# Kernel optimization log

Measured on AMD Instinct MI355X. Metric: run time of the kernel, lower is better.

## Reference

```python
import jax, jax.numpy as jnp
import numpy as np

EPS = 1e-5
NUM_GROUPS = 32
NUM_HEADS = 8

def group_norm(x, w, b):
    # x: (B, C, H, W), 32 groups, affine per-channel
    B, C, H, W = x.shape
    xg = x.reshape(B, NUM_GROUPS, C // NUM_GROUPS, H, W)
    mu = xg.mean(axis=(2, 3, 4), keepdims=True)
    var = xg.var(axis=(2, 3, 4), keepdims=True)
    xn = ((xg - mu) * jax.lax.rsqrt(var + EPS)).reshape(B, C, H, W)
    return xn * w[None, :, None, None] + b[None, :, None, None]

def conv1x1(x, w, b):
    # 1x1 conv == per-pixel linear; w: (out, in), x: (B, C, H, W)
    return jnp.einsum('oc,bchw->bohw', w, x) + b[None, :, None, None]

def setup_inputs() -> dict:
    key = jax.random.key(0)
    ks = jax.random.split(key, 4)
    B, C, H, W = 2, 512, 64, 64
    s = 1.0 / np.sqrt(C)
    return {
        'x': jax.random.normal(ks[0], (B, C, H, W), jnp.float32),
        'gn_w': jnp.ones((C,), jnp.float32),
        'gn_b': jnp.zeros((C,), jnp.float32),
        'wq': jax.random.normal(ks[1], (C, C), jnp.float32) * s,
        'bq': jnp.zeros((C,), jnp.float32),
        'wkv': jax.random.normal(ks[2], (2 * C, C), jnp.float32) * s,
        'bkv': jnp.zeros((2 * C,), jnp.float32),
        'wo': jax.random.normal(ks[3], (C, C), jnp.float32) * s,
        'bo': jnp.zeros((C,), jnp.float32),
    }

def reference(x, gn_w, gn_b, wq, bq, wkv, bkv, wo, bo):
    B, C, H, W = x.shape
    hd = C // NUM_HEADS  # head_dim
    residual = x
    x_norm = group_norm(x, gn_w, gn_b)
    q = conv1x1(x_norm, wq, bq).reshape(B, NUM_HEADS, hd, H * W)
    kv = conv1x1(x_norm, wkv, bkv)
    k, v = jnp.split(kv, 2, axis=1)
    k = k.reshape(B, NUM_HEADS, hd, H * W)
    v = v.reshape(B, NUM_HEADS, hd, H * W)
    scale = hd ** (-0.5)
    attn = jnp.einsum('bhdi,bhdj->bhij', q, k) * scale
    attn = jax.nn.softmax(attn, axis=-1)
    out = jnp.einsum('bhij,bhdj->bhdi', attn, v).reshape(B, C, H, W)
    out = conv1x1(out, wo, bo)
    return out + residual
```

## Files before the change

kernel.cpp:

```cpp
#include <hip/hip_runtime.h>
#include <cmath>

typedef __bf16 bf16x8 __attribute__((ext_vector_type(8)));
typedef __bf16 bf16x4 __attribute__((ext_vector_type(4)));
typedef float  f32x4  __attribute__((ext_vector_type(4)));

static __device__ __forceinline__ f32x4 mfma16(bf16x8 a, bf16x8 b, f32x4 c) {
    return __builtin_amdgcn_mfma_f32_16x16x32_bf16(a, b, c, 0, 0, 0);
}

static __device__ __forceinline__ float fast_exp2(float x) {
#if __has_builtin(__builtin_amdgcn_exp2f)
    return __builtin_amdgcn_exp2f(x);
#else
    return exp2f(x);
#endif
}

#define OFF_STATS 0
#define OFF_W     4096
#define OFF_XNT   (OFF_W + 2u*1024*1024)
#define OFF_QKT   (OFF_XNT + 8u*1024*1024)
#define OFF_V     (OFF_QKT + 16u*1024*1024)
#define OFF_OP    (OFF_V + 8u*1024*1024)
#define OFF_LP    (OFF_OP + 32u*1024*1024)

__global__ __launch_bounds__(256) void cvt_w(const float* __restrict__ wq,
                                             const float* __restrict__ wkv,
                                             const float* __restrict__ wo,
                                             __bf16* __restrict__ dst) {
    int i = blockIdx.x * 256 + threadIdx.x;
    if (i < 262144)      dst[i] = (__bf16)wq[i];
    else if (i < 786432) dst[i] = (__bf16)wkv[i - 262144];
    else                 dst[i] = (__bf16)wo[i - 786432];
}

__global__ __launch_bounds__(256) void gn_stats(const float* __restrict__ x,
                                                float* __restrict__ stats) {
    int blk = blockIdx.x;
    int bg = blk >> 2, chunk = blk & 3;
    const float* base = x + (size_t)bg * 65536 + (size_t)chunk * 16384;
    float s = 0.f, ss = 0.f;
    for (int i = threadIdx.x; i < 4096; i += 256) {
        float4 v = ((const float4*)base)[i];
        s  += v.x + v.y + v.z + v.w;
        ss += v.x*v.x + v.y*v.y + v.z*v.z + v.w*v.w;
    }
    #pragma unroll
    for (int off = 1; off < 64; off <<= 1) {
        s  += __shfl_xor(s,  off);
        ss += __shfl_xor(ss, off);
    }
    __shared__ float red[8];
    int wave = threadIdx.x >> 6;
    if ((threadIdx.x & 63) == 0) { red[wave*2] = s; red[wave*2+1] = ss; }
    __syncthreads();
    if (threadIdx.x == 0) {
        float S  = red[0] + red[2] + red[4] + red[6];
        float SS = red[1] + red[3] + red[5] + red[7];
        atomicAdd(&stats[bg*2],     S);
        atomicAdd(&stats[bg*2 + 1], SS);
    }
}

__global__ __launch_bounds__(256) void gn_apply(const float* __restrict__ x,
                                                const float* __restrict__ stats,
                                                const float* __restrict__ w,
                                                const float* __restrict__ bgn,
                                                __bf16* __restrict__ xnT) {
    int p0 = blockIdx.x * 64, c0 = blockIdx.y * 64, b = blockIdx.z;
    int tid = threadIdx.x, lane = tid & 63, wave = tid >> 6;
    __shared__ float t[64][69];
    #pragma unroll
    for (int i = 0; i < 16; ++i) {
        int cc = i * 4 + wave;
        int c  = c0 + cc;
        int g  = (b << 5) + (c >> 4);
        float mu  = stats[g*2] * (1.f/65536.f);
        float var = stats[g*2+1] * (1.f/65536.f) - mu*mu;
        float rstd = rsqrtf(var + 1e-5f);
        float val = x[((size_t)(b*512 + c) << 12) + p0 + lane];
        t[cc][lane] = (val - mu) * rstd * w[c] + bgn[c];
    }
    __syncthreads();
    #pragma unroll
    for (int i = 0; i < 16; ++i) {
        int pp = i * 4 + wave;
        xnT[((size_t)(b*4096 + p0 + pp) << 9) + c0 + lane] = (__bf16)t[lane][pp];
    }
}

__global__ __launch_bounds__(256) void gemm128_kernel(
    const __bf16* __restrict__ A, const __bf16* __restrict__ B,
    const float* __restrict__ bias, const float* __restrict__ bias2, int nsplit,
    float scale0, void* __restrict__ out,
    int N, int K, long long strideA, long long strideO) {
    const int bz = blockIdx.z;
    A += strideA * bz;
    const int m0 = blockIdx.x * 128, n0 = blockIdx.y * 128;
    const int tid = threadIdx.x, lane = tid & 63, wave = tid >> 6;
    const int quad = lane >> 4, l16 = lane & 15;
    const int wm = (wave >> 1) * 64, wn = (wave & 1) * 64;

    __shared__ __attribute__((aligned(16))) __bf16 lds_a[128][40];
    __shared__ __attribute__((aligned(16))) __bf16 lds_b[128][40];

    f32x4 acc[4][4];
    #pragma unroll
    for (int mt = 0; mt < 4; ++mt)
        #pragma unroll
        for (int nt = 0; nt < 4; ++nt)
            #pragma unroll
            for (int r = 0; r < 4; ++r) acc[mt][nt][r] = 0.f;

    const int row_s = tid >> 2;
    const int kc    = (tid & 3) << 3;

    uint4 ra0, ra1, rb0, rb1;
    const __bf16* Abase = A + (size_t)(m0 + row_s) * K + kc;
    const __bf16* Bbase = B + (size_t)(n0 + row_s) * K + kc;
    ra0 = *(const uint4*)Abase;
    ra1 = *(const uint4*)(Abase + (size_t)64 * K);
    rb0 = *(const uint4*)Bbase;
    rb1 = *(const uint4*)(Bbase + (size_t)64 * K);

    for (int kt = 0; kt < K; kt += 32) {
        *(uint4*)&lds_a[row_s][kc]      = ra0;
        *(uint4*)&lds_a[row_s + 64][kc] = ra1;
        *(uint4*)&lds_b[row_s][kc]      = rb0;
        *(uint4*)&lds_b[row_s + 64][kc] = rb1;
        __syncthreads();
        if (kt + 32 < K) {
            ra0 = *(const uint4*)(Abase + kt + 32);
            ra1 = *(const uint4*)(Abase + kt + 32 + (size_t)64 * K);
            rb0 = *(const uint4*)(Bbase + kt + 32);
            rb1 = *(const uint4*)(Bbase + kt + 32 + (size_t)64 * K);
        }
        bf16x8 af[4], bfr[4];
        #pragma unroll
        for (int mt = 0; mt < 4; ++mt)
            af[mt] = *(const bf16x8*)&lds_a[wm + mt*16 + l16][quad*8];
        #pragma unroll
        for (int nt = 0; nt < 4; ++nt)
            bfr[nt] = *(const bf16x8*)&lds_b[wn + nt*16 + l16][quad*8];
        #pragma unroll
        for (int mt = 0; mt < 4; ++mt)
            #pragma unroll
            for (int nt = 0; nt < 4; ++nt)
                acc[mt][nt] = mfma16(af[mt], bfr[nt], acc[mt][nt]);
        __syncthreads();
    }

    #pragma unroll
    for (int mt = 0; mt < 4; ++mt) {
        const int mrow = m0 + wm + mt*16 + quad*4;
        #pragma unroll
        for (int nt = 0; nt < 4; ++nt) {
            const int ncol = n0 + wn + nt*16 + l16;
            #pragma unroll
            for (int r = 0; r < 4; ++r) {
                const int m = mrow + r;
                float bval = (ncol < nsplit) ? bias[ncol] : bias2[ncol - nsplit];
                float val = acc[mt][nt][r] + bval;
                if (ncol < nsplit) val *= scale0;
                ((__bf16*)out)[(size_t)strideO * bz + (size_t)m * N + ncol] = (__bf16)val;
            }
        }
    }
}

template<int OUT_F32, int HAS_RES>
__global__ __launch_bounds__(256) void gemm64_kernel(
    const __bf16* __restrict__ A, const __bf16* __restrict__ B,
    const float* __restrict__ bias, const float* __restrict__ res,
    void* __restrict__ out,
    int N, int K, long long strideB, long long strideO) {
    const int bz = blockIdx.z;
    B += strideB * bz;
    const int m0 = blockIdx.x * 64, n0 = blockIdx.y * 128;
    const int tid = threadIdx.x, lane = tid & 63, wave = tid >> 6;
    const int quad = lane >> 4, l16 = lane & 15;
    const int wn = wave * 32;

    __shared__ __attribute__((aligned(16))) __bf16 lds_a[64][40];
    __shared__ __attribute__((aligned(16))) __bf16 lds_b[128][40];

    f32x4 acc[4][2];
    #pragma unroll
    for (int mt = 0; mt < 4; ++mt)
        #pragma unroll
        for (int nt = 0; nt < 2; ++nt)
            #pragma unroll
            for (int r = 0; r < 4; ++r) acc[mt][nt][r] = 0.f;

    const int row_s = tid >> 2;
    const int kc    = (tid & 3) << 3;

    uint4 ra0, rb0, rb1;
    const __bf16* Abase = A + (size_t)(m0 + row_s) * K + kc;
    const __bf16* Bbase = B + (size_t)(n0 + row_s) * K + kc;
    ra0 = *(const uint4*)Abase;
    rb0 = *(const uint4*)Bbase;
    rb1 = *(const uint4*)(Bbase + (size_t)64 * K);

    for (int kt = 0; kt < K; kt += 32) {
        *(uint4*)&lds_a[row_s][kc]      = ra0;
        *(uint4*)&lds_b[row_s][kc]      = rb0;
        *(uint4*)&lds_b[row_s + 64][kc] = rb1;
        __syncthreads();
        if (kt + 32 < K) {
            ra0 = *(const uint4*)(Abase + kt + 32);
            rb0 = *(const uint4*)(Bbase + kt + 32);
            rb1 = *(const uint4*)(Bbase + kt + 32 + (size_t)64 * K);
        }
        bf16x8 af[4], bfr[2];
        #pragma unroll
        for (int mt = 0; mt < 4; ++mt)
            af[mt] = *(const bf16x8*)&lds_a[mt*16 + l16][quad*8];
        #pragma unroll
        for (int nt = 0; nt < 2; ++nt)
            bfr[nt] = *(const bf16x8*)&lds_b[wn + nt*16 + l16][quad*8];
        #pragma unroll
        for (int mt = 0; mt < 4; ++mt)
            #pragma unroll
            for (int nt = 0; nt < 2; ++nt)
                acc[mt][nt] = mfma16(af[mt], bfr[nt], acc[mt][nt]);
        __syncthreads();
    }

    #pragma unroll
    for (int mt = 0; mt < 4; ++mt) {
        const int mrow = m0 + mt*16 + quad*4;
        #pragma unroll
        for (int nt = 0; nt < 2; ++nt) {
            const int ncol = n0 + wn + nt*16 + l16;
            #pragma unroll
            for (int r = 0; r < 4; ++r) {
                const int m = mrow + r;
                float val = acc[mt][nt][r] + bias[m];
                const size_t idx = (size_t)strideO * bz + (size_t)m * N + ncol;
                if constexpr (HAS_RES) val += res[idx];
                if constexpr (OUT_F32) ((float*)out)[idx] = val;
                else ((__bf16*)out)[idx] = (__bf16)val;
            }
        }
    }
}

template<int SPLIT>
__global__ __launch_bounds__(256) void attn_kernel(const __bf16* __restrict__ qkT,
                                                   const __bf16* __restrict__ v,
                                                   __bf16* __restrict__ attnT,
                                                   float* __restrict__ Opart,
                                                   float* __restrict__ Lpart) {
    const int b = blockIdx.y >> 3, h = blockIdx.y & 7;
    const int chunk = SPLIT ? blockIdx.z : 0;
    const int NITER = SPLIT ? 32 : 64;
    const int kt0 = chunk * (SPLIT ? 2048 : 4096);
    const int tid = threadIdx.x;
    const int wave = tid >> 6, lane = tid & 63;
    const int quad = lane >> 4, l16 = lane & 15;
    const int qbase = blockIdx.x * 256 + wave * 64;

    const __bf16* qkTb = qkT + ((size_t)b << 22);
    const __bf16* vb   = v   + ((size_t)b << 21);

    __shared__ __attribute__((aligned(16))) __bf16 lds_k[2][64][64];
    __shared__ __attribute__((aligned(16))) __bf16 lds_v[2][64][64];
    __shared__ __attribute__((aligned(16))) __bf16 lds_p[4][64][72];

    bf16x8 aq[4][2];
    #pragma unroll
    for (int mt = 0; mt < 4; ++mt) {
        const __bf16* qrow = qkTb + (size_t)(qbase + mt*16 + l16) * 1024 + h*64 + quad*8;
        aq[mt][0] = *(const bf16x8*)qrow;
        aq[mt][1] = *(const bf16x8*)(qrow + 32);
    }
    f32x4 o[4][4];
    float lsum[4][4];
    #pragma unroll
    for (int mt = 0; mt < 4; ++mt) {
        #pragma unroll
        for (int r = 0; r < 4; ++r) lsum[mt][r] = 0.f;
        #pragma unroll
        for (int dt = 0; dt < 4; ++dt)
            #pragma unroll
            for (int r = 0; r < 4; ++r) o[mt][dt][r] = 0.f;
    }

    const int srow = tid >> 2;
    const int sc   = tid & 3;
    const int sw0  = ( sc      ^ (srow & 7)) * 8;
    const int sw1  = ((sc + 4) ^ (srow & 7)) * 8;

    const __bf16* kg0 = qkTb + (size_t)srow * 1024 + 512 + h*64 + sc*8;
    const __bf16* vg0 = vb + ((size_t)(h*64 + srow) << 12) + sc*8;

    {
        const __bf16* kg = kg0 + (size_t)kt0 * 1024;
        const __bf16* vg = vg0 + kt0;
        *(uint4*)&lds_k[0][srow][sw0] = *(const uint4*)kg;
        *(uint4*)&lds_k[0][srow][sw1] = *(const uint4*)(kg + 32);
        *(uint4*)&lds_v[0][srow][sw0] = *(const uint4*)vg;
        *(uint4*)&lds_v[0][srow][sw1] = *(const uint4*)(vg + 32);
    }
    __syncthreads();

    for (int it = 0; it < NITER; ++it) {
        const int cur = it & 1, nxt = cur ^ 1;
        uint4 ck0, ck1, cv0, cv1;
        if (it + 1 < NITER) {
            const int kt = kt0 + (it + 1) * 64;
            const __bf16* kg = kg0 + (size_t)kt * 1024;
            const __bf16* vg = vg0 + kt;
            ck0 = *(const uint4*)kg; ck1 = *(const uint4*)(kg + 32);
            cv0 = *(const uint4*)vg; cv1 = *(const uint4*)(vg + 32);
        }

        #pragma unroll
        for (int nt = 0; nt < 4; ++nt) {
            const int kr = nt*16 + l16;
            bf16x8 bk0 = *(const bf16x8*)&lds_k[cur][kr][( quad      ^ (l16 & 7)) * 8];
            bf16x8 bk1 = *(const bf16x8*)&lds_k[cur][kr][((4 + quad) ^ (l16 & 7)) * 8];
            #pragma unroll
            for (int mt = 0; mt < 4; ++mt) {
                f32x4 s;
                #pragma unroll
                for (int r = 0; r < 4; ++r) s[r] = 0.f;
                s = mfma16(aq[mt][0], bk0, s);
                s = mfma16(aq[mt][1], bk1, s);
                f32x4 p;
                #pragma unroll
                for (int r = 0; r < 4; ++r) {
                    p[r] = fast_exp2(s[r]);
                    lsum[mt][r] += p[r];
                }
                bf16x4 pb = __builtin_convertvector(p, bf16x4);
                #pragma unroll
                for (int r = 0; r < 4; ++r)
                    lds_p[wave][mt*16 + quad*4 + r][nt*16 + l16] = pb[r];
            }
        }

        #pragma unroll
        for (int kc = 0; kc < 2; ++kc) {
            bf16x8 pa[4];
            #pragma unroll
            for (int mt = 0; mt < 4; ++mt)
                pa[mt] = *(const bf16x8*)&lds_p[wave][mt*16 + l16][kc*32 + quad*8];
            #pragma unroll
            for (int dt = 0; dt < 4; ++dt) {
                bf16x8 bv = *(const bf16x8*)&lds_v[cur][dt*16 + l16][((kc*4 + quad) ^ (l16 & 7)) * 8];
                #pragma unroll
                for (int mt = 0; mt < 4; ++mt)
                    o[mt][dt] = mfma16(pa[mt], bv, o[mt][dt]);
            }
        }

        if (it + 1 < NITER) {
            *(uint4*)&lds_k[nxt][srow][sw0] = ck0;
            *(uint4*)&lds_k[nxt][srow][sw1] = ck1;
            *(uint4*)&lds_v[nxt][srow][sw0] = cv0;
            *(uint4*)&lds_v[nxt][srow][sw1] = cv1;
        }
        __syncthreads();
    }

    float lred[4][4];
    #pragma unroll
    for (int mt = 0; mt < 4; ++mt)
        #pragma unroll
        for (int r = 0; r < 4; ++r) {
            float s = lsum[mt][r];
            s += __shfl_xor(s, 1);
            s += __shfl_xor(s, 2);
            s += __shfl_xor(s, 4);
            s += __shfl_xor(s, 8);
            lred[mt][r] = s;
        }

    if constexpr (SPLIT) {
        float* Ob = Opart + (size_t)chunk * 4194304;
        #pragma unroll
        for (int mt = 0; mt < 4; ++mt)
            #pragma unroll
            for (int dt = 0; dt < 4; ++dt)
                #pragma unroll
                for (int r = 0; r < 4; ++r) {
                    size_t row = (size_t)b * 4096 + qbase + mt*16 + quad*4 + r;
                    Ob[(row << 9) + (h << 6) + dt*16 + l16] = o[mt][dt][r];
                }
        if (l16 == 0) {
            #pragma unroll
            for (int mt = 0; mt < 4; ++mt)
                #pragma unroll
                for (int r = 0; r < 4; ++r) {
                    int p = qbase + mt*16 + quad*4 + r;
                    Lpart[(size_t)(((chunk*2 + b)*8 + h) << 12) + p] = lred[mt][r];
                }
        }
    } else {
        #pragma unroll
        for (int mt = 0; mt < 4; ++mt)
            #pragma unroll
            for (int dt = 0; dt < 4; ++dt)
                #pragma unroll
                for (int r = 0; r < 4; ++r) {
                    size_t row = (size_t)b * 4096 + qbase + mt*16 + quad*4 + r;
                    attnT[(row << 9) + (h << 6) + dt*16 + l16] =
                        (__bf16)(o[mt][dt][r] / lred[mt][r]);
                }
    }
}

__global__ __launch_bounds__(256) void attn_combine(const float* __restrict__ Opart,
                                                    const float* __restrict__ Lpart,
                                                    __bf16* __restrict__ attnT) {
    int i = blockIdx.x * 256 + threadIdx.x;
    int c4 = i & 127;
    int p  = (i >> 7) & 4095;
    int b  = i >> 19;
    int h  = c4 >> 4;
    size_t lidx = (size_t)((b*8 + h) << 12) + p;
    float l = Lpart[lidx] + Lpart[lidx + 65536];
    float inv = 1.f / l;
    size_t oi = ((size_t)(b*4096 + p) << 7) + c4;
    float4 o0 = ((const float4*)Opart)[oi];
    float4 o1 = ((const float4*)Opart)[oi + 1048576];
    bf16x4 rv;
    rv[0] = (__bf16)((o0.x + o1.x) * inv);
    rv[1] = (__bf16)((o0.y + o1.y) * inv);
    rv[2] = (__bf16)((o0.z + o1.z) * inv);
    rv[3] = (__bf16)((o0.w + o1.w) * inv);
    *(bf16x4*)&attnT[oi << 2] = rv;
}

extern "C" void kernel_launch(void* const* d_in, const int* in_sizes, int n_in,
                              void* d_out, int out_size, void* d_ws, size_t ws_size,
                              hipStream_t stream) {
    const float* x   = (const float*)d_in[0];
    const float* gnw = (const float*)d_in[1];
    const float* gnb = (const float*)d_in[2];
    const float* wq  = (const float*)d_in[3];
    const float* bq  = (const float*)d_in[4];
    const float* wkv = (const float*)d_in[5];
    const float* bkv = (const float*)d_in[6];
    const float* wo  = (const float*)d_in[7];
    const float* bo  = (const float*)d_in[8];
    float* out = (float*)d_out;

    char* ws = (char*)d_ws;
    float*  stats  = (float*)(ws + OFF_STATS);
    __bf16* wbf    = (__bf16*)(ws + OFF_W);
    __bf16* wkv_bf = wbf + 262144;
    __bf16* wo_bf  = wbf + 786432;
    __bf16* xnT    = (__bf16*)(ws + OFF_XNT);
    __bf16* qkT    = (__bf16*)(ws + OFF_QKT);
    __bf16* vv     = (__bf16*)(ws + OFF_V);
    float*  Opart  = (float*)(ws + OFF_OP);
    float*  Lpart  = (float*)(ws + OFF_LP);
    __bf16* attnT  = xnT;

    const bool split = ws_size >= (size_t)OFF_LP + 524288u;

    hipMemsetAsync(stats, 0, 512, stream);
    cvt_w<<<4096, 256, 0, stream>>>(wq, wkv, wo, wbf);
    gn_stats<<<256, 256, 0, stream>>>(x, stats);
    gn_apply<<<dim3(64, 8, 2), 256, 0, stream>>>(x, stats, gnw, gnb, xnT);

    const long long S = 2097152LL;
    const long long S2 = 4194304LL;
    gemm128_kernel<<<dim3(32, 8, 2), 256, 0, stream>>>(
        xnT, wbf, bq, bkv, 512, 0.125f * 1.44269504f, qkT, 1024, 512, S, S2);
    gemm64_kernel<0,0><<<dim3(8, 32, 2), 256, 0, stream>>>(
        wkv_bf + 262144, xnT, bkv + 512, nullptr, vv, 4096, 512, S, S);

    if (split) {
        attn_kernel<1><<<dim3(16, 16, 2), 256, 0, stream>>>(qkT, vv, nullptr, Opart, Lpart);
        attn_combine<<<4096, 256, 0, stream>>>(Opart, Lpart, attnT);
    } else {
        attn_kernel<0><<<dim3(16, 16, 1), 256, 0, stream>>>(qkT, vv, attnT, nullptr, nullptr);
    }

    gemm64_kernel<1,1><<<dim3(8, 32, 2), 256, 0, stream>>>(
        wo_bf, attnT, bo, x, out, 4096, 512, S, S);
}
```

Before: 242.3 us.

## Split attention over four KV chunks, fold row-sum into MFMA, single-buffer LDS

The attention kernel can now split the KV range into 4 chunks when the workspace is large enough, up from 2. The softmax row sum is computed by an extra MFMA against a row of ones in the V tile, replacing per-element adds and the shuffle reduction. K/V LDS goes from double-buffered to single-buffered with register prefetch, and partial outputs are stored in bf16 instead of fp32. Launch bounds request 3 blocks per CU. These aim at occupancy, parallelism and partial-output traffic, at the cost of bf16 rounding in the partials, an extra combine pass and one more MFMA column per step.

```diff
diff --git a/kernel.cpp b/kernel.cpp
--- a/kernel.cpp
+++ b/kernel.cpp
@@ -23,7 +23,8 @@
 #define OFF_QKT   (OFF_XNT + 8u*1024*1024)
 #define OFF_V     (OFF_QKT + 16u*1024*1024)
 #define OFF_OP    (OFF_V + 8u*1024*1024)
-#define OFF_LP    (OFF_OP + 32u*1024*1024)
+#define CHUNK_O   4194304u
+#define CHUNK_L   65536u
 
 __global__ __launch_bounds__(256) void cvt_w(const float* __restrict__ wq,
                                              const float* __restrict__ wkv,
@@ -247,16 +248,16 @@
     }
 }
 
-template<int SPLIT>
-__global__ __launch_bounds__(256) void attn_kernel(const __bf16* __restrict__ qkT,
-                                                   const __bf16* __restrict__ v,
-                                                   __bf16* __restrict__ attnT,
-                                                   float* __restrict__ Opart,
-                                                   float* __restrict__ Lpart) {
+template<int NCH>
+__global__ __launch_bounds__(256, 3) void attn_kernel(const __bf16* __restrict__ qkT,
+                                                      const __bf16* __restrict__ v,
+                                                      __bf16* __restrict__ attnT,
+                                                      __bf16* __restrict__ Opart,
+                                                      float* __restrict__ Lpart) {
     const int b = blockIdx.y >> 3, h = blockIdx.y & 7;
-    const int chunk = SPLIT ? blockIdx.z : 0;
-    const int NITER = SPLIT ? 32 : 64;
-    const int kt0 = chunk * (SPLIT ? 2048 : 4096);
+    const int chunk = (NCH > 1) ? blockIdx.z : 0;
+    const int NITER = 64 / NCH;
+    const int kt0 = chunk * (4096 / NCH);
     const int tid = threadIdx.x;
     const int wave = tid >> 6, lane = tid & 63;
     const int quad = lane >> 4, l16 = lane & 15;
@@ -265,9 +266,9 @@
     const __bf16* qkTb = qkT + ((size_t)b << 22);
     const __bf16* vb   = v   + ((size_t)b << 21);
 
-    __shared__ __attribute__((aligned(16))) __bf16 lds_k[2][64][64];
-    __shared__ __attribute__((aligned(16))) __bf16 lds_v[2][64][64];
-    __shared__ __attribute__((aligned(16))) __bf16 lds_p[4][64][72];
+    __shared__ __attribute__((aligned(16))) __bf16 lds_k[64][64];
+    __shared__ __attribute__((aligned(16))) __bf16 lds_v[80][64];
+    __shared__ __attribute__((aligned(16))) __bf16 lds_p[4][64][68];
 
     bf16x8 aq[4][2];
     #pragma unroll
@@ -276,17 +277,14 @@
         aq[mt][0] = *(const bf16x8*)qrow;
         aq[mt][1] = *(const bf16x8*)(qrow + 32);
     }
-    f32x4 o[4][4];
-    float lsum[4][4];
-    #pragma unroll
-    for (int mt = 0; mt < 4; ++mt) {
-        #pragma unroll
-        for (int r = 0; r < 4; ++r) lsum[mt][r] = 0.f;
-        #pragma unroll
-        for (int dt = 0; dt < 4; ++dt)
+    f32x4 o[4][5];
+    #pragma unroll
+    for (int mt = 0; mt < 4; ++mt)
+        #pragma unroll
+        for (int dt = 0; dt < 5; ++dt)
             #pragma unroll
             for (int r = 0; r < 4; ++r) o[mt][dt][r] = 0.f;
-    }
+    const f32x4 kZero = {0.f, 0.f, 0.f, 0.f};
 
     const int srow = tid >> 2;
     const int sc   = tid & 3;
@@ -296,19 +294,22 @@
     const __bf16* kg0 = qkTb + (size_t)srow * 1024 + 512 + h*64 + sc*8;
     const __bf16* vg0 = vb + ((size_t)(h*64 + srow) << 12) + sc*8;
 
+    if (tid < 64) lds_v[64][tid] = (__bf16)1.0f;
+
+    uint4 ck0, ck1, cv0, cv1;
     {
         const __bf16* kg = kg0 + (size_t)kt0 * 1024;
         const __bf16* vg = vg0 + kt0;
-        *(uint4*)&lds_k[0][srow][sw0] = *(const uint4*)kg;
-        *(uint4*)&lds_k[0][srow][sw1] = *(const uint4*)(kg + 32);
-        *(uint4*)&lds_v[0][srow][sw0] = *(const uint4*)vg;
-        *(uint4*)&lds_v[0][srow][sw1] = *(const uint4*)(vg + 32);
-    }
-    __syncthreads();
+        ck0 = *(const uint4*)kg; ck1 = *(const uint4*)(kg + 32);
+        cv0 = *(const uint4*)vg; cv1 = *(const uint4*)(vg + 32);
+    }
 
     for (int it = 0; it < NITER; ++it) {
-        const int cur = it & 1, nxt = cur ^ 1;
-        uint4 ck0, ck1, cv0, cv1;
+        *(uint4*)&lds_k[srow][sw0] = ck0;
+        *(uint4*)&lds_k[srow][sw1] = ck1;
+        *(uint4*)&lds_v[srow][sw0] = cv0;
+        *(uint4*)&lds_v[srow][sw1] = cv1;
+        __syncthreads();
         if (it + 1 < NITER) {
             const int kt = kt0 + (it + 1) * 64;
             const __bf16* kg = kg0 + (size_t)kt * 1024;
@@ -320,25 +321,16 @@
         #pragma unroll
         for (int nt = 0; nt < 4; ++nt) {
             const int kr = nt*16 + l16;
-            bf16x8 bk0 = *(const bf16x8*)&lds_k[cur][kr][( quad      ^ (l16 & 7)) * 8];
-            bf16x8 bk1 = *(const bf16x8*)&lds_k[cur][kr][((4 + quad) ^ (l16 & 7)) * 8];
+            bf16x8 bk0 = *(const bf16x8*)&lds_k[kr][( quad      ^ (l16 & 7)) * 8];
+            bf16x8 bk1 = *(const bf16x8*)&lds_k[kr][((4 + quad) ^ (l16 & 7)) * 8];
             #pragma unroll
             for (int mt = 0; mt < 4; ++mt) {
-                f32x4 s;
-                #pragma unroll
-                for (int r = 0; r < 4; ++r) s[r] = 0.f;
-                s = mfma16(aq[mt][0], bk0, s);
-                s = mfma16(aq[mt][1], bk1, s);
+                f32x4 s = mfma16(bk1, aq[mt][1], mfma16(bk0, aq[mt][0], kZero));
                 f32x4 p;
                 #pragma unroll
-                for (int r = 0; r < 4; ++r) {
-                    p[r] = fast_exp2(s[r]);
-                    lsum[mt][r] += p[r];
-                }
+                for (int r = 0; r < 4; ++r) p[r] = fast_exp2(s[r]);
                 bf16x4 pb = __builtin_convertvector(p, bf16x4);
-                #pragma unroll
-                for (int r = 0; r < 4; ++r)
-                    lds_p[wave][mt*16 + quad*4 + r][nt*16 + l16] = pb[r];
+                *(bf16x4*)&lds_p[wave][mt*16 + l16][nt*16 + quad*4] = pb;
             }
         }
 
@@ -346,41 +338,24 @@
         for (int kc = 0; kc < 2; ++kc) {
             bf16x8 pa[4];
             #pragma unroll
-            for (int mt = 0; mt < 4; ++mt)
-                pa[mt] = *(const bf16x8*)&lds_p[wave][mt*16 + l16][kc*32 + quad*8];
-            #pragma unroll
-            for (int dt = 0; dt < 4; ++dt) {
-                bf16x8 bv = *(const bf16x8*)&lds_v[cur][dt*16 + l16][((kc*4 + quad) ^ (l16 & 7)) * 8];
+            for (int mt = 0; mt < 4; ++mt) {
+                bf16x4 plo = *(const bf16x4*)&lds_p[wave][mt*16 + l16][kc*32 + quad*8];
+                bf16x4 phi = *(const bf16x4*)&lds_p[wave][mt*16 + l16][kc*32 + quad*8 + 4];
+                pa[mt] = __builtin_shufflevector(plo, phi, 0, 1, 2, 3, 4, 5, 6, 7);
+            }
+            #pragma unroll
+            for (int dt = 0; dt < 5; ++dt) {
+                bf16x8 bv = *(const bf16x8*)&lds_v[dt*16 + l16][((kc*4 + quad) ^ (l16 & 7)) * 8];
                 #pragma unroll
                 for (int mt = 0; mt < 4; ++mt)
                     o[mt][dt] = mfma16(pa[mt], bv, o[mt][dt]);
             }
         }
-
-        if (it + 1 < NITER) {
-            *(uint4*)&lds_k[nxt][srow][sw0] = ck0;
-            *(uint4*)&lds_k[nxt][srow][sw1] = ck1;
-            *(uint4*)&lds_v[nxt][srow][sw0] = cv0;
-            *(uint4*)&lds_v[nxt][srow][sw1] = cv1;
-        }
-        __syncthreads();
-    }
-
-    float lred[4][4];
-    #pragma unroll
-    for (int mt = 0; mt < 4; ++mt)
-        #pragma unroll
-        for (int r = 0; r < 4; ++r) {
-            float s = lsum[mt][r];
-            s += __shfl_xor(s, 1);
-            s += __shfl_xor(s, 2);
-            s += __shfl_xor(s, 4);
-            s += __shfl_xor(s, 8);
-            lred[mt][r] = s;
-        }
-
-    if constexpr (SPLIT) {
-        float* Ob = Opart + (size_t)chunk * 4194304;
+        __syncthreads();
+    }
+
+    if constexpr (NCH > 1) {
+        __bf16* Ob = Opart + (size_t)chunk * CHUNK_O;
         #pragma unroll
         for (int mt = 0; mt < 4; ++mt)
             #pragma unroll
@@ -388,7 +363,7 @@
                 #pragma unroll
                 for (int r = 0; r < 4; ++r) {
                     size_t row = (size_t)b * 4096 + qbase + mt*16 + quad*4 + r;
-                    Ob[(row << 9) + (h << 6) + dt*16 + l16] = o[mt][dt][r];
+                    Ob[(row << 9) + (h << 6) + dt*16 + l16] = (__bf16)o[mt][dt][r];
                 }
         if (l16 == 0) {
             #pragma unroll
@@ -396,24 +371,29 @@
                 #pragma unroll
                 for (int r = 0; r < 4; ++r) {
                     int p = qbase + mt*16 + quad*4 + r;
-                    Lpart[(size_t)(((chunk*2 + b)*8 + h) << 12) + p] = lred[mt][r];
+                    Lpart[(size_t)chunk * CHUNK_L + (size_t)(((b*8 + h)) << 12) + p] = o[mt][4][r];
                 }
         }
     } else {
         #pragma unroll
-        for (int mt = 0; mt < 4; ++mt)
+        for (int mt = 0; mt < 4; ++mt) {
+            float inv[4];
+            #pragma unroll
+            for (int r = 0; r < 4; ++r)
+                inv[r] = 1.f / __shfl(o[mt][4][r], lane & 48);
             #pragma unroll
             for (int dt = 0; dt < 4; ++dt)
                 #pragma unroll
                 for (int r = 0; r < 4; ++r) {
                     size_t row = (size_t)b * 4096 + qbase + mt*16 + quad*4 + r;
-                    attnT[(row << 9) + (h << 6) + dt*16 + l16] =
-                        (__bf16)(o[mt][dt][r] / lred[mt][r]);
+                    attnT[(row << 9) + (h << 6) + dt*16 + l16] = (__bf16)(o[mt][dt][r] * inv[r]);
                 }
-    }
-}
-
-__global__ __launch_bounds__(256) void attn_combine(const float* __restrict__ Opart,
+        }
+    }
+}
+
+template<int NCH>
+__global__ __launch_bounds__(256) void attn_combine(const __bf16* __restrict__ Opart,
                                                     const float* __restrict__ Lpart,
                                                     __bf16* __restrict__ attnT) {
     int i = blockIdx.x * 256 + threadIdx.x;
@@ -422,17 +402,22 @@
     int b  = i >> 19;
     int h  = c4 >> 4;
     size_t lidx = (size_t)((b*8 + h) << 12) + p;
-    float l = Lpart[lidx] + Lpart[lidx + 65536];
+    float l = 0.f;
+    #pragma unroll
+    for (int ch = 0; ch < NCH; ++ch) l += Lpart[(size_t)ch * CHUNK_L + lidx];
     float inv = 1.f / l;
-    size_t oi = ((size_t)(b*4096 + p) << 7) + c4;
-    float4 o0 = ((const float4*)Opart)[oi];
-    float4 o1 = ((const float4*)Opart)[oi + 1048576];
+    size_t oi = ((size_t)(b*4096 + p) << 9) + c4*4;
+    float acc[4] = {0.f, 0.f, 0.f, 0.f};
+    #pragma unroll
+    for (int ch = 0; ch < NCH; ++ch) {
+        bf16x4 ov = *(const bf16x4*)&Opart[(size_t)ch * CHUNK_O + oi];
+        #pragma unroll
+        for (int r = 0; r < 4; ++r) acc[r] += (float)ov[r];
+    }
     bf16x4 rv;
-    rv[0] = (__bf16)((o0.x + o1.x) * inv);
-    rv[1] = (__bf16)((o0.y + o1.y) * inv);
-    rv[2] = (__bf16)((o0.z + o1.z) * inv);
-    rv[3] = (__bf16)((o0.w + o1.w) * inv);
-    *(bf16x4*)&attnT[oi << 2] = rv;
+    #pragma unroll
+    for (int r = 0; r < 4; ++r) rv[r] = (__bf16)(acc[r] * inv);
+    *(bf16x4*)&attnT[oi] = rv;
 }
 
 extern "C" void kernel_launch(void* const* d_in, const int* in_sizes, int n_in,
@@ -457,11 +442,13 @@
     __bf16* xnT    = (__bf16*)(ws + OFF_XNT);
     __bf16* qkT    = (__bf16*)(ws + OFF_QKT);
     __bf16* vv     = (__bf16*)(ws + OFF_V);
-    float*  Opart  = (float*)(ws + OFF_OP);
-    float*  Lpart  = (float*)(ws + OFF_LP);
+    __bf16* Opart  = (__bf16*)(ws + OFF_OP);
     __bf16* attnT  = xnT;
 
-    const bool split = ws_size >= (size_t)OFF_LP + 524288u;
+    const size_t need4 = (size_t)OFF_OP + 4u * (CHUNK_O * 2 + CHUNK_L * 4);
+    const size_t need2 = (size_t)OFF_OP + 2u * (CHUNK_O * 2 + CHUNK_L * 4);
+    const int nch = (ws_size >= need4) ? 4 : (ws_size >= need2 ? 2 : 1);
+    float* Lpart = (float*)(ws + OFF_OP + (size_t)nch * CHUNK_O * 2);
 
     hipMemsetAsync(stats, 0, 512, stream);
     cvt_w<<<4096, 256, 0, stream>>>(wq, wkv, wo, wbf);
@@ -475,11 +462,14 @@
     gemm64_kernel<0,0><<<dim3(8, 32, 2), 256, 0, stream>>>(
         wkv_bf + 262144, xnT, bkv + 512, nullptr, vv, 4096, 512, S, S);
 
-    if (split) {
-        attn_kernel<1><<<dim3(16, 16, 2), 256, 0, stream>>>(qkT, vv, nullptr, Opart, Lpart);
-        attn_combine<<<4096, 256, 0, stream>>>(Opart, Lpart, attnT);
+    if (nch == 4) {
+        attn_kernel<4><<<dim3(16, 16, 4), 256, 0, stream>>>(qkT, vv, nullptr, Opart, Lpart);
+        attn_combine<4><<<4096, 256, 0, stream>>>(Opart, Lpart, attnT);
+    } else if (nch == 2) {
+        attn_kernel<2><<<dim3(16, 16, 2), 256, 0, stream>>>(qkT, vv, nullptr, Opart, Lpart);
+        attn_combine<2><<<4096, 256, 0, stream>>>(Opart, Lpart, attnT);
     } else {
-        attn_kernel<0><<<dim3(16, 16, 1), 256, 0, stream>>>(qkT, vv, attnT, nullptr, nullptr);
+        attn_kernel<1><<<dim3(16, 16, 1), 256, 0, stream>>>(qkT, vv, attnT, nullptr, nullptr);
     }
 
     gemm64_kernel<1,1><<<dim3(8, 32, 2), 256, 0, stream>>>(
```

Result: faster. 229.3 us (-5.3%).
